# Kernel optimization log

Measured on AMD Instinct MI355X. Metric: run time of the kernel, lower is better.

Reference implementation:

```python
import jax, jax.numpy as jnp
import numpy as np

PAD_ID = 1
NEG = jnp.float32(-1e30)


def setup_inputs() -> dict:
    key = jax.random.key(0)
    ks = jax.random.split(key, 12)
    T, B, S, D, E, V = 20, 32, 400, 512, 512, 50000
    s = 0.02  # weight init scale for numerical sanity
    return {
        "inputs": jax.random.randint(ks[0], (T, B), 0, V),
        "src": jax.random.randint(ks[1], (S, B, 1), 0, V),
        "h_e": jax.random.normal(ks[2], (S, B, D), jnp.float32),
        "h0": jnp.zeros((B, D), jnp.float32),
        "c0": jnp.zeros((B, D), jnp.float32),
        "W_emb": jax.random.normal(ks[3], (V, E), jnp.float32) * s,
        "W_proj": jax.random.normal(ks[4], (E, 3 * D), jnp.float32) * s,
        "b_out": jax.random.normal(ks[5], (V,), jnp.float32) * s,
        "proj_u_W": jax.random.normal(ks[6], (1, 3 * D), jnp.float32) * s,
        "proj_u_b": jnp.zeros((1,), jnp.float32),
        "enc_W": jax.random.normal(ks[7], (D, D), jnp.float32) * s,
        "dec_W": jax.random.normal(ks[8], (D, D), jnp.float32) * s,
        "W_ih": jax.random.normal(ks[9], (4 * D, E), jnp.float32) * s,
        "W_hh": jax.random.normal(ks[10], (4 * D, D), jnp.float32) * s,
        "b_ih": jnp.zeros((4 * D,), jnp.float32),
        "b_hh": jnp.zeros((4 * D,), jnp.float32),
    }


def reference(inputs, src, h_e, h0, c0, W_emb, W_proj, b_out, proj_u_W,
              proj_u_b, enc_W, dec_W, W_ih, W_hh, b_ih, b_hh):
    T, B = inputs.shape
    D = h0.shape[1]
    V = W_emb.shape[0]
    src_bs = src[:, :, 0].T                       # [B, S]
    # Sect 2.4 shared output weights: W_out = tanh(W_emb @ W_proj)  [V, 3D]
    W_out = jnp.tanh(W_emb @ W_proj)
    rows = jnp.arange(B)[:, None]
    tpos = jnp.arange(T)

    def step(carry, xs):
        h, c, hist = carry                        # hist: [T, B, D] decoder-state history
        inp_t, t = xs
        emb = W_emb[inp_t]                        # [B, E]
        # single-layer LSTM cell (torch gate order i, f, g, o)
        gates = emb @ W_ih.T + h @ W_hh.T + b_ih + b_hh
        i, f, g, o = jnp.split(gates, 4, axis=-1)
        c_new = jax.nn.sigmoid(f) * c + jax.nn.sigmoid(i) * jnp.tanh(g)
        hd = jax.nn.sigmoid(o) * jnp.tanh(c_new)  # [B, D]
        # encoder intra-attention
        q = hd @ enc_W.T
        ae = jax.nn.softmax(jnp.einsum('bd,sbd->bs', q, h_e), axis=-1)  # [B, S]
        ce = jnp.einsum('bs,sbd->bd', ae, h_e)
        # decoder intra-attention over steps < t (zero context at t==0)
        qd = hd @ dec_W.T
        sd = jnp.einsum('bd,tbd->bt', qd, hist)
        sd = jnp.where(tpos[None, :] < t, sd, NEG)
        ad = jax.nn.softmax(sd, axis=-1)
        cd = jnp.where(t > 0, jnp.einsum('bt,tbd->bd', ad, hist), 0.0)
        hist = hist.at[t].set(hd)
        # pointer-generator
        ccat = jnp.concatenate([hd, ce, cd], axis=-1)        # [B, 3D]
        logits = ccat @ W_out.T + b_out                      # [B, V]
        logits = logits.at[:, PAD_ID].set(NEG)
        p_gen = jax.nn.softmax(logits, axis=-1)
        p_switch = jax.nn.sigmoid(ccat @ proj_u_W.T + proj_u_b)  # [B, 1]
        # copy distribution: scatter attention into vocab
        copy = jnp.zeros((B, V), logits.dtype).at[rows, src_bs].add(ae)
        scores = copy * p_switch + p_gen * (1.0 - p_switch)
        return (hd, c_new, hist), scores

    hist0 = jnp.zeros((T, B, D), h0.dtype)
    _, scores = jax.lax.scan(step, (h0, c0, hist0), (inputs, tpos))
    return scores  # [T, B, V]
```

## Files before the change

### kernel.cpp

```cpp
#include <hip/hip_runtime.h>
#include <stdint.h>

typedef unsigned short u16;
typedef unsigned int   u32;

using f32x4 = __attribute__((ext_vector_type(4))) float;
using s16x8 = __attribute__((ext_vector_type(8))) short;

#define TT 20
#define BB 32
#define SS 400
#define DD 512
#define VV 50000
#define VP2 50176

__device__ __forceinline__ float bf2f(u16 u){
  u32 x = ((u32)u) << 16;
  return __builtin_bit_cast(float, x);
}
__device__ __forceinline__ u16 f2bf(float f){
  u32 x = __builtin_bit_cast(u32, f);
  x = x + 0x7fffu + ((x >> 16) & 1u);
  return (u16)(x >> 16);
}
__device__ __forceinline__ float sigm(float x){ return 1.0f/(1.0f + __expf(-x)); }
__device__ __forceinline__ float tanh_fast(float x){
  float a = fabsf(x);
  if (a < 0.25f){ float x2 = x*x; return x + x*x2*(-0.33333334f + 0.13333334f*x2); }
  return tanhf(x);
}
__device__ __forceinline__ void gld16(const void* g, void* l){
  __builtin_amdgcn_global_load_lds((const __attribute__((address_space(1))) void*)g,
                                   (__attribute__((address_space(3))) void*)l, 16, 0, 0);
}

__global__ __launch_bounds__(256) void k_prep(
    const float* __restrict__ W_proj,
    const float* __restrict__ W_ih,   const float* __restrict__ W_hh,
    const float* __restrict__ b_ih,   const float* __restrict__ b_hh,
    const float* __restrict__ h0,     const float* __restrict__ c0,
    const float* __restrict__ enc_W,  const float* __restrict__ dec_W,
    u16* __restrict__ WpT,
    u16* __restrict__ Wihs, u16* __restrict__ Whhs,
    u16* __restrict__ encWb, u16* __restrict__ decWb, float* __restrict__ bgs,
    float* __restrict__ hist, u16* __restrict__ histb, float* __restrict__ c_st,
    float* __restrict__ psE)
{
  int i = blockIdx.x*256 + threadIdx.x;
  if (i < 1280){ psE[i] = 0.0f; return; }
  i -= 1280;
  if (i < 2048){ int d = i >> 2, g = i & 3; bgs[i] = b_ih[g*512 + d] + b_hh[g*512 + d]; return; }
  i -= 2048;
  if (i < 16384){ float hv = h0[i]; hist[i] = hv; histb[i] = f2bf(hv); c_st[i] = c0[i]; return; }
  i -= 16384;
  if (i < 786432){ int j = i >> 9, k = i & 511; WpT[i] = f2bf(W_proj[k*1536 + j]); return; }
  i -= 786432;
  if (i < 1048576){
    int mp = i >> 9, k = i & 511; int d = mp >> 2, g = mp & 3;
    Wihs[i] = f2bf(W_ih[(size_t)(g*512 + d)*512 + k]); return; }
  i -= 1048576;
  if (i < 1048576){
    int mp = i >> 9, k = i & 511; int d = mp >> 2, g = mp & 3;
    Whhs[i] = f2bf(W_hh[(size_t)(g*512 + d)*512 + k]); return; }
  i -= 1048576;
  if (i < 262144){ encWb[i] = f2bf(enc_W[i]); return; }
  i -= 262144;
  if (i < 262144){ decWb[i] = f2bf(dec_W[i]); return; }
}

__global__ __launch_bounds__(256) void k_cast_emb(const float* __restrict__ in, u16* __restrict__ out){
  int i = blockIdx.x*256 + threadIdx.x;
  int base = i*4;
  if (base >= VP2*DD) return;
  uint2 o;
  if (base < VV*DD){
    float4 v = *(const float4*)&in[base];
    o.x = (u32)f2bf(v.x) | ((u32)f2bf(v.y) << 16);
    o.y = (u32)f2bf(v.z) | ((u32)f2bf(v.w) << 16);
  } else { o.x = 0u; o.y = 0u; }
  *(uint2*)&out[base] = o;
}

__global__ __launch_bounds__(256) void k_cast_he(const float* __restrict__ in, u16* __restrict__ out){
  int i = blockIdx.x*256 + threadIdx.x;
  int base = i*4;
  if (base >= SS*BB*DD) return;
  const int s = base >> 14;
  const int b = (base >> 9) & 31;
  const int d = base & 511;
  float4 v = *(const float4*)&in[base];
  uint2 o;
  o.x = (u32)f2bf(v.x) | ((u32)f2bf(v.y) << 16);
  o.y = (u32)f2bf(v.z) | ((u32)f2bf(v.w) << 16);
  *(uint2*)&out[((size_t)(b*SS + s) << 9) + d] = o;
}

__global__ __launch_bounds__(256) void k_gather(const int* __restrict__ inp,
                                                const u16* __restrict__ Wb, u16* __restrict__ out){
  int i = blockIdx.x*256 + threadIdx.x;
  if (i >= TT*BB*DD) return;
  int r = i >> 9, k = i & 511;
  out[i] = Wb[(size_t)inp[r]*DD + k];
}

template<int EPI>
__device__ __forceinline__ void gemm_tile(
    const u16* __restrict__ A, const u16* __restrict__ B,
    float* __restrict__ Cf, u16* __restrict__ Cb, const float* __restrict__ bias,
    int K, int mt, int nt, int ldc, int nmax, char* smemc)
{
  u16* As = (u16*)smemc;
  u16* Bs = (u16*)(smemc + 16384);
  const int tid = threadIdx.x;
  const int w = tid >> 6, l = tid & 63;
  const int m0 = mt*128, n0 = nt*128;
  const int srow = tid >> 3;
  const int scol = ((tid & 7) ^ ((tid >> 3) & 7)) * 8;
  const int wm = (w >> 1)*64, wn = (w & 1)*64;
  const int fr = l & 15;
  const int g4 = l >> 4;
  f32x4 acc[4][4] = {};
  for (int k0 = 0; k0 < K; k0 += 64){
    #pragma unroll
    for (int j = 0; j < 4; ++j){
      gld16(A + (size_t)(m0 + j*32 + srow)*K + k0 + scol, (char*)As + j*4096 + (w << 10));
      gld16(B + (size_t)(n0 + j*32 + srow)*K + k0 + scol, (char*)Bs + j*4096 + (w << 10));
    }
    __syncthreads();
    #pragma unroll
    for (int h = 0; h < 2; ++h){
      s16x8 af[4], bfr[4];
      #pragma unroll
      for (int i = 0; i < 4; ++i){
        const int ra = wm + i*16 + fr;
        af[i]  = *(const s16x8*)((char*)As + ra*128 + ((((h << 2) + g4) ^ (ra & 7)) << 4));
        const int rb = wn + i*16 + fr;
        bfr[i] = *(const s16x8*)((char*)Bs + rb*128 + ((((h << 2) + g4) ^ (rb & 7)) << 4));
      }
      #pragma unroll
      for (int i = 0; i < 4; ++i)
        #pragma unroll
        for (int j2 = 0; j2 < 4; ++j2)
          acc[i][j2] = __builtin_amdgcn_mfma_f32_16x16x32_bf16(af[i], bfr[j2], acc[i][j2], 0, 0, 0);
    }
    __syncthreads();
  }
  #pragma unroll
  for (int i = 0; i < 4; ++i){
    #pragma unroll
    for (int j = 0; j < 4; ++j){
      #pragma unroll
      for (int r = 0; r < 4; ++r){
        const int row = m0 + wm + i*16 + (l >> 4)*4 + r;
        const int col = n0 + wn + j*16 + fr;
        const float v = acc[i][j][r];
        if constexpr (EPI == 0){ Cf[(size_t)row*ldc + col] = v; }
        else if constexpr (EPI == 1){ Cb[(size_t)row*ldc + col] = f2bf(tanh_fast(v)); }
        else { if (col < nmax) Cb[(size_t)row*ldc + col] = f2bf(v + bias[col]); }
      }
    }
  }
}

template<int EPI, int ORD>
__global__ __launch_bounds__(256) void gemm_bt(
    const u16* __restrict__ A, const u16* __restrict__ B,
    float* __restrict__ Cf, u16* __restrict__ Cb, const float* __restrict__ bias,
    int K, int TM, int TN, int ldc, int nmax)
{
  __shared__ __align__(16) char smem[32768];
  int bid = blockIdx.x;
  if (ORD >= 1){
    const int n = TM*TN, x = bid & 7, i = bid >> 3;
    const int q = n >> 3, r = n & 7;
    bid = (x < r ? x*(q+1) : r*(q+1) + (x-r)*q) + i;
  }
  const int mt = (ORD == 1) ? bid / TN : bid % TM;
  const int nt = (ORD == 1) ? bid % TN : bid / TM;
  gemm_tile<EPI>(A, B, Cf, Cb, bias, K, mt, nt, ldc, nmax, smem);
}

__global__ __launch_bounds__(256) void k_lstm(
    const u16* __restrict__ Whhs, const float* __restrict__ X, const float* __restrict__ bgs,
    float* __restrict__ hist, u16* __restrict__ histb, float* __restrict__ c_st,
    u16* __restrict__ ccatb, int t)
{
  __shared__ __align__(16) u16 Hs[32*512];
  __shared__ __align__(16) u16 As[16*512];
  __shared__ float Cp[4][16][32];
  const int blk = blockIdx.x;
  const int tid = threadIdx.x;
  const int w = tid >> 6, l = tid & 63;
  const char* hsrc = (const char*)(histb + (size_t)t*16384);
  #pragma unroll
  for (int p = 0; p < 8; ++p)
    gld16(hsrc + p*4096 + w*1024 + l*16, (char*)Hs + p*4096 + w*1024);
  const char* asrc = (const char*)(Whhs + (size_t)blk*16*512);
  #pragma unroll
  for (int p = 0; p < 4; ++p)
    gld16(asrc + p*4096 + w*1024 + l*16, (char*)As + p*4096 + w*1024);
  __syncthreads();
  {
    const int fr = l & 15, fko = (l >> 4)*8;
    f32x4 acc0 = {}, acc1 = {};
    #pragma unroll
    for (int kk = 0; kk < 4; ++kk){
      const int kb = (w*4 + kk)*32;
      s16x8 af = *(const s16x8*)&As[fr*512 + kb + fko];
      s16x8 b0 = *(const s16x8*)&Hs[fr*512 + kb + fko];
      s16x8 b1 = *(const s16x8*)&Hs[(16 + fr)*512 + kb + fko];
      acc0 = __builtin_amdgcn_mfma_f32_16x16x32_bf16(af, b0, acc0, 0, 0, 0);
      acc1 = __builtin_amdgcn_mfma_f32_16x16x32_bf16(af, b1, acc1, 0, 0, 0);
    }
    #pragma unroll
    for (int r = 0; r < 4; ++r){
      Cp[w][(l >> 4)*4 + r][fr]      = acc0[r];
      Cp[w][(l >> 4)*4 + r][16 + fr] = acc1[r];
    }
  }
  __syncthreads();
  if (tid < 128){
    const int dl = tid >> 5, b = tid & 31;
    const int d = blk*4 + dl;
    const int bd = b*512 + d;
    float gv[4];
    #pragma unroll
    for (int g = 0; g < 4; ++g)
      gv[g] = Cp[0][dl*4 + g][b] + Cp[1][dl*4 + g][b] + Cp[2][dl*4 + g][b] + Cp[3][dl*4 + g][b];
    const float4 x4 = *(const float4*)&X[((size_t)(t*BB + b))*2048 + d*4];
    const float4 g4 = *(const float4*)&bgs[d*4];
    const float iv = gv[0] + x4.x + g4.x;
    const float fv = gv[1] + x4.y + g4.y;
    const float gg = gv[2] + x4.z + g4.z;
    const float ov = gv[3] + x4.w + g4.w;
    const float cn = sigm(fv)*c_st[bd] + sigm(iv)*tanhf(gg);
    const float hd = sigm(ov)*tanhf(cn);
    c_st[bd] = cn;
    hist[(size_t)(t + 1)*16384 + bd] = hd;
    const u16 hb = f2bf(hd);
    histb[(size_t)(t + 1)*16384 + bd] = hb;
    ccatb[((size_t)(t*BB + b))*1536 + d] = hb;
  }
}

__global__ __launch_bounds__(256) void k_bulkq(
    const u16* __restrict__ Hb, const u16* __restrict__ encWb, const u16* __restrict__ decWb,
    float* __restrict__ qe_all, float* __restrict__ qd_all)
{
  __shared__ __align__(16) char smem[32768];
  const int e = blockIdx.x;
  const int which = e / 20;
  const int e2 = e % 20;
  const int mt = e2 % 5, nt = e2 / 5;
  gemm_tile<0>(Hb, which ? decWb : encWb, which ? qd_all : qe_all,
               nullptr, nullptr, 512, mt, nt, 512, 0, smem);
}

__global__ __launch_bounds__(256) void k_attn(
    const u16* __restrict__ heb, const float* __restrict__ hist,
    const float* __restrict__ qe_all, const float* __restrict__ qd_all,
    const float* __restrict__ puW,
    u16* __restrict__ ccatb, float* __restrict__ aeall,
    float* __restrict__ psE, float* __restrict__ psD)
{
  __shared__ float hcur[512];
  __shared__ float qv[512];
  __shared__ float ael[SS];
  __shared__ float red[256];
  __shared__ float part[4*512];
  __shared__ float adl[TT];
  __shared__ float sdl[TT];
  __shared__ float shs[2];
  const int blk = blockIdx.x;
  const int tid = threadIdx.x;

  if (blk < 640){
    const int row = blk;
    const int t = row >> 5, b = row & 31;
    const float* hsrc = hist + (size_t)(t + 1)*16384 + b*512;
    const float* qsrc = qe_all + (size_t)row*512;
    hcur[tid] = hsrc[tid]; hcur[tid + 256] = hsrc[tid + 256];
    qv[tid] = qsrc[tid];   qv[tid + 256] = qsrc[tid + 256];
    __syncthreads();
    for (int pass = 0; pass < 7; ++pass){
      const int s = pass*64 + (tid >> 2);
      if (s < SS){
        const u16* gp = heb + ((size_t)(b*SS + s))*512 + (tid & 3)*128;
        const float* hp = qv + (tid & 3)*128;
        float p = 0.0f;
        #pragma unroll 4
        for (int k8 = 0; k8 < 128; k8 += 8){
          s16x8 g8 = *(const s16x8*)&gp[k8];
          #pragma unroll
          for (int q = 0; q < 8; ++q) p += bf2f((u16)g8[q])*hp[k8 + q];
        }
        p += __shfl_xor(p, 1); p += __shfl_xor(p, 2);
        if ((tid & 3) == 0) ael[s] = p;
      }
    }
    __syncthreads();
    float lm = -1e30f;
    for (int s = tid; s < SS; s += 256) lm = fmaxf(lm, ael[s]);
    red[tid] = lm; __syncthreads();
    for (int st = 128; st; st >>= 1){ if (tid < st) red[tid] = fmaxf(red[tid], red[tid + st]); __syncthreads(); }
    const float M = red[0]; __syncthreads();
    float ls = 0.0f;
    for (int s = tid; s < SS; s += 256){ float p = __expf(ael[s] - M); ael[s] = p; ls += p; }
    red[tid] = ls; __syncthreads();
    for (int st = 128; st; st >>= 1){ if (tid < st) red[tid] += red[tid + st]; __syncthreads(); }
    const float inv = 1.0f/red[0];
    __syncthreads();
    {
      const int g = tid >> 6, th = tid & 63;
      const int d0 = th*8;
      float a8[8] = {};
      for (int s = g; s < SS; s += 4){
        const float a = ael[s];
        s16x8 hv = *(const s16x8*)&heb[((size_t)(b*SS + s))*512 + d0];
        #pragma unroll
        for (int q = 0; q < 8; ++q) a8[q] += a*bf2f((u16)hv[q]);
      }
      *(float4*)&part[g*512 + d0]     = float4{a8[0], a8[1], a8[2], a8[3]};
      *(float4*)&part[g*512 + d0 + 4] = float4{a8[4], a8[5], a8[6], a8[7]};
    }
    __syncthreads();
    {
      const int dd = tid*2;
      float ce0 = part[dd]     + part[512 + dd]     + part[1024 + dd]     + part[1536 + dd];
      float ce1 = part[dd + 1] + part[512 + dd + 1] + part[1024 + dd + 1] + part[1536 + dd + 1];
      ce0 *= inv; ce1 *= inv;
      *(u32*)&ccatb[(size_t)row*1536 + 512 + dd] = (u32)f2bf(ce0) | ((u32)f2bf(ce1) << 16);
      float pv = hcur[dd]*puW[dd] + hcur[dd + 1]*puW[dd + 1]
               + ce0*puW[512 + dd] + ce1*puW[512 + dd + 1];
      red[tid] = pv;
    }
    __syncthreads();
    for (int st = 128; st; st >>= 1){ if (tid < st) red[tid] += red[tid + st]; __syncthreads(); }
    if (tid == 0) psE[row] = red[0];
    for (int s = tid; s < SS; s += 256) aeall[(size_t)row*SS + s] = ael[s]*inv;
  } else {
    const int row = blk - 640;
    const int t = row >> 5, b = row & 31;
    const float* qsrc = qd_all + (size_t)row*512;
    qv[tid] = qsrc[tid]; qv[tid + 256] = qsrc[tid + 256];
    __syncthreads();
    for (int u0 = 0; u0 < t; u0 += 8){
      const int u = u0 + (tid >> 5);
      if (u < t){
        const float* hu = hist + (size_t)(u + 1)*16384 + b*512;
        float p = 0.0f;
        #pragma unroll
        for (int j = 0; j < 4; ++j){
          const int kb = (tid & 31)*4 + j*128;
          const float4 h4 = *(const float4*)&hu[kb];
          const float4 q4 = *(const float4*)&qv[kb];
          p += h4.x*q4.x + h4.y*q4.y + h4.z*q4.z + h4.w*q4.w;
        }
        p += __shfl_xor(p, 1); p += __shfl_xor(p, 2); p += __shfl_xor(p, 4);
        p += __shfl_xor(p, 8); p += __shfl_xor(p, 16);
        if ((tid & 31) == 0) sdl[u] = p;
      }
    }
    __syncthreads();
    if (tid == 0 && t > 0){
      float m2 = -1e30f;
      for (int u = 0; u < t; ++u) m2 = fmaxf(m2, sdl[u]);
      float s2 = 0.0f;
      for (int u = 0; u < t; ++u){ float p = __expf(sdl[u] - m2); adl[u] = p; s2 += p; }
      shs[0] = 1.0f/s2;
    }
    __syncthreads();
    const float invd = (t > 0) ? shs[0] : 0.0f;
    const int d0 = tid*2;
    float e0 = 0.0f, e1 = 0.0f;
    for (int u = 0; u < t; ++u){
      const float a = adl[u];
      const float* hu = hist + (size_t)(u + 1)*16384 + b*512 + d0;
      e0 += a*hu[0]; e1 += a*hu[1];
    }
    e0 *= invd; e1 *= invd;
    *(u32*)&ccatb[(size_t)row*1536 + 1024 + d0] = (u32)f2bf(e0) | ((u32)f2bf(e1) << 16);
    float pv = e0*puW[1024 + d0] + e1*puW[1024 + d0 + 1];
    red[tid] = pv; __syncthreads();
    for (int st = 128; st; st >>= 1){ if (tid < st) red[tid] += red[tid + st]; __syncthreads(); }
    if (tid == 0) psD[row] = red[0];
  }
}

__global__ __launch_bounds__(256) void k_softmax(
    const u16* __restrict__ lg, float* __restrict__ out,
    const float* __restrict__ psE, const float* __restrict__ psD, const float* __restrict__ puB,
    const int* __restrict__ src, const float* __restrict__ ae_all)
{
  const int r = blockIdx.x, tid = threadIdx.x;
  __shared__ float rm[256], rs[256];
  const u16* row = lg + (size_t)r*VP2;
  float m = -1e30f, s = 0.0f;
  for (int v8 = tid*8; v8 < VV; v8 += 2048){
    uint4 pk = *(const uint4*)&row[v8];
    u32 wds[4] = {pk.x, pk.y, pk.z, pk.w};
    #pragma unroll
    for (int q = 0; q < 8; ++q){
      if (v8 + q == 1) continue;
      float x = bf2f((u16)((wds[q >> 1] >> ((q & 1)*16)) & 0xffffu));
      if (x > m){ s = s*__expf(m - x) + 1.0f; m = x; }
      else s += __expf(x - m);
    }
  }
  rm[tid] = m; rs[tid] = s; __syncthreads();
  for (int st = 128; st; st >>= 1){
    if (tid < st){
      float m2 = fmaxf(rm[tid], rm[tid + st]);
      rs[tid] = rs[tid]*__expf(rm[tid] - m2) + rs[tid + st]*__expf(rm[tid + st] - m2);
      rm[tid] = m2;
    }
    __syncthreads();
  }
  const float M = rm[0];
  const float ps = 1.0f/(1.0f + __expf(-(psE[r] + psD[r] + puB[0])));
  const float inv = (1.0f - ps)/rs[0];
  float* orow = out + (size_t)r*VV;
  for (int v8 = tid*8; v8 < VV; v8 += 2048){
    uint4 pk = *(const uint4*)&row[v8];
    u32 wds[4] = {pk.x, pk.y, pk.z, pk.w};
    float o[8];
    #pragma unroll
    for (int q = 0; q < 8; ++q){
      float x = bf2f((u16)((wds[q >> 1] >> ((q & 1)*16)) & 0xffffu));
      o[q] = (v8 + q == 1) ? 0.0f : __expf(x - M)*inv;
    }
    *(float4*)&orow[v8]     = float4{o[0], o[1], o[2], o[3]};
    *(float4*)&orow[v8 + 4] = float4{o[4], o[5], o[6], o[7]};
  }
  __syncthreads();
  const int b = r & 31;
  for (int sp = tid; sp < SS; sp += 256){
    const int v = src[sp*BB + b];
    atomicAdd(&orow[v], ae_all[(size_t)r*SS + sp]*ps);
  }
}

extern "C" void kernel_launch(void* const* d_in, const int* in_sizes, int n_in,
                              void* d_out, int out_size, void* d_ws, size_t ws_size,
                              hipStream_t stream)
{
  const int*   inputs = (const int*)  d_in[0];
  const int*   src    = (const int*)  d_in[1];
  const float* h_e    = (const float*)d_in[2];
  const float* h0     = (const float*)d_in[3];
  const float* c0     = (const float*)d_in[4];
  const float* W_emb  = (const float*)d_in[5];
  const float* W_proj = (const float*)d_in[6];
  const float* b_out  = (const float*)d_in[7];
  const float* puW    = (const float*)d_in[8];
  const float* puB    = (const float*)d_in[9];
  const float* enc_W  = (const float*)d_in[10];
  const float* dec_W  = (const float*)d_in[11];
  const float* W_ih   = (const float*)d_in[12];
  const float* W_hh   = (const float*)d_in[13];
  const float* b_ih   = (const float*)d_in[14];
  const float* b_hh   = (const float*)d_in[15];
  float* out = (float*)d_out;

  char* wp = (char*)d_ws;
  auto alloc = [&](size_t bytes) -> char* {
    char* p = wp; wp += (bytes + 255) & ~(size_t)255; return p;
  };
  u16*   Wembb = (u16*)  alloc((size_t)VP2*DD*2);
  u16*   WpT   = (u16*)  alloc(1536*512*2);
  u16*   heb   = (u16*)  alloc((size_t)SS*BB*DD*2);
  u16*   logitsb = (u16*)Wembb;
  u16*   Woutb = (u16*)  alloc((size_t)VP2*1536*2);
  u16*   Wihs  = (u16*)  alloc(2048*512*2);
  u16*   Whhs  = (u16*)  alloc(2048*512*2);
  u16*   encWb = (u16*)  alloc(512*512*2);
  u16*   decWb = (u16*)  alloc(512*512*2);
  float* bgs   = (float*)alloc(2048*4);
  u16*   emba  = (u16*)  alloc((size_t)TT*BB*DD*2);
  float* X     = (float*)alloc((size_t)TT*BB*2048*4);
  float* c_st  = (float*)alloc(BB*DD*4);
  float* hist  = (float*)alloc((size_t)(TT+1)*BB*DD*4);
  u16*   histb = (u16*)  alloc((size_t)(TT+1)*BB*DD*2);
  u16*   ccatb = (u16*)  alloc((size_t)TT*BB*1536*2);
  float* aeall = (float*)alloc((size_t)TT*BB*SS*4);
  float* psE   = (float*)alloc(1280*4);
  float* psD   = psE + 640;
  float* qe_all= (float*)alloc((size_t)TT*BB*DD*4);
  float* qd_all= (float*)alloc((size_t)TT*BB*DD*4);

  k_prep<<<13389, 256, 0, stream>>>(W_proj, W_ih, W_hh, b_ih, b_hh, h0, c0, enc_W, dec_W,
                                    WpT, Wihs, Whhs, encWb, decWb, bgs, hist, histb, c_st, psE);
  k_cast_emb<<<(VP2*DD/4)/256, 256, 0, stream>>>(W_emb, Wembb);
  k_cast_he<<<(SS*BB*DD/4)/256, 256, 0, stream>>>(h_e, heb);
  k_gather<<<(TT*BB*DD + 255)/256, 256, 0, stream>>>(inputs, Wembb, emba);

  gemm_bt<0,0><<<5*16, 256, 0, stream>>>(emba, Wihs, X, nullptr, nullptr, 512, 5, 16, 2048, 0);

  gemm_bt<1,1><<<392*12, 256, 0, stream>>>(Wembb, WpT, nullptr, Woutb, nullptr, 512, 392, 12, 1536, 0);

  for (int t = 0; t < TT; ++t)
    k_lstm<<<128, 256, 0, stream>>>(Whhs, X, bgs, hist, histb, c_st, ccatb, t);

  k_bulkq<<<40, 256, 0, stream>>>(histb + 16384, encWb, decWb, qe_all, qd_all);
  k_attn<<<1280, 256, 0, stream>>>(heb, hist, qe_all, qd_all, puW, ccatb, aeall, psE, psD);

  gemm_bt<3,2><<<5*392, 256, 0, stream>>>(ccatb, Woutb, nullptr, logitsb, b_out, 1536, 5, 392, VP2, VV);

  k_softmax<<<TT*BB, 256, 0, stream>>>(logitsb, out, psE, psD, puB, src, aeall);
}
```

Baseline: 508.3 us.

## Merge prep cast kernels into one launch and stage GEMM epilogue through LDS

Folds the embedding cast, encoder-state cast/transpose and token gather into the single prep kernel. The gather now reads fp32 W_emb directly, so it no longer depends on the cast output. The bf16 GEMM epilogues now write results into shared memory first, then emit 16-byte coalesced row stores, with the bias hoisted into registers. This is meant to cut launch overhead and the scattered 2-byte global stores on the large vocab-output and W_out GEMMs, at the cost of extra LDS (34816 bytes per block) and an additional barrier.

```diff
diff --git a/kernel.cpp b/kernel.cpp
--- a/kernel.cpp
+++ b/kernel.cpp
@@ -40,11 +40,14 @@
     const float* __restrict__ b_ih,   const float* __restrict__ b_hh,
     const float* __restrict__ h0,     const float* __restrict__ c0,
     const float* __restrict__ enc_W,  const float* __restrict__ dec_W,
+    const float* __restrict__ W_emb,  const float* __restrict__ h_e,
+    const int*   __restrict__ inputs,
     u16* __restrict__ WpT,
     u16* __restrict__ Wihs, u16* __restrict__ Whhs,
     u16* __restrict__ encWb, u16* __restrict__ decWb, float* __restrict__ bgs,
     float* __restrict__ hist, u16* __restrict__ histb, float* __restrict__ c_st,
-    float* __restrict__ psE)
+    float* __restrict__ psE,
+    u16* __restrict__ Wembb, u16* __restrict__ heb, u16* __restrict__ emba)
 {
   int i = blockIdx.x*256 + threadIdx.x;
   if (i < 1280){ psE[i] = 0.0f; return; }
@@ -66,41 +69,39 @@
   if (i < 262144){ encWb[i] = f2bf(enc_W[i]); return; }
   i -= 262144;
   if (i < 262144){ decWb[i] = f2bf(dec_W[i]); return; }
-}
-
-__global__ __launch_bounds__(256) void k_cast_emb(const float* __restrict__ in, u16* __restrict__ out){
-  int i = blockIdx.x*256 + threadIdx.x;
-  int base = i*4;
-  if (base >= VP2*DD) return;
-  uint2 o;
-  if (base < VV*DD){
-    float4 v = *(const float4*)&in[base];
+  i -= 262144;
+  if (i < 6422528){
+    int base = i*4;
+    uint2 o;
+    if (base < VV*DD){
+      float4 v = *(const float4*)&W_emb[base];
+      o.x = (u32)f2bf(v.x) | ((u32)f2bf(v.y) << 16);
+      o.y = (u32)f2bf(v.z) | ((u32)f2bf(v.w) << 16);
+    } else { o.x = 0u; o.y = 0u; }
+    *(uint2*)&Wembb[base] = o;
+    return; }
+  i -= 6422528;
+  if (i < 1638400){
+    int base = i*4;
+    const int s = base >> 14;
+    const int b = (base >> 9) & 31;
+    const int d = base & 511;
+    float4 v = *(const float4*)&h_e[base];
+    uint2 o;
     o.x = (u32)f2bf(v.x) | ((u32)f2bf(v.y) << 16);
     o.y = (u32)f2bf(v.z) | ((u32)f2bf(v.w) << 16);
-  } else { o.x = 0u; o.y = 0u; }
-  *(uint2*)&out[base] = o;
-}
-
-__global__ __launch_bounds__(256) void k_cast_he(const float* __restrict__ in, u16* __restrict__ out){
-  int i = blockIdx.x*256 + threadIdx.x;
-  int base = i*4;
-  if (base >= SS*BB*DD) return;
-  const int s = base >> 14;
-  const int b = (base >> 9) & 31;
-  const int d = base & 511;
-  float4 v = *(const float4*)&in[base];
-  uint2 o;
-  o.x = (u32)f2bf(v.x) | ((u32)f2bf(v.y) << 16);
-  o.y = (u32)f2bf(v.z) | ((u32)f2bf(v.w) << 16);
-  *(uint2*)&out[((size_t)(b*SS + s) << 9) + d] = o;
-}
-
-__global__ __launch_bounds__(256) void k_gather(const int* __restrict__ inp,
-                                                const u16* __restrict__ Wb, u16* __restrict__ out){
-  int i = blockIdx.x*256 + threadIdx.x;
-  if (i >= TT*BB*DD) return;
-  int r = i >> 9, k = i & 511;
-  out[i] = Wb[(size_t)inp[r]*DD + k];
+    *(uint2*)&heb[((size_t)(b*SS + s) << 9) + d] = o;
+    return; }
+  i -= 1638400;
+  if (i < 81920){
+    int base = i*4;
+    int r = base >> 9, k = base & 511;
+    float4 v = *(const float4*)&W_emb[(size_t)inputs[r]*DD + k];
+    uint2 o;
+    o.x = (u32)f2bf(v.x) | ((u32)f2bf(v.y) << 16);
+    o.y = (u32)f2bf(v.z) | ((u32)f2bf(v.w) << 16);
+    *(uint2*)&emba[base] = o;
+    return; }
 }
 
 template<int EPI>
@@ -119,6 +120,14 @@
   const int wm = (w >> 1)*64, wn = (w & 1)*64;
   const int fr = l & 15;
   const int g4 = l >> 4;
+  float bv[4];
+  if constexpr (EPI == 3){
+    #pragma unroll
+    for (int j = 0; j < 4; ++j){
+      const int c = n0 + wn + j*16 + fr;
+      bv[j] = (c < nmax) ? bias[c] : 0.0f;
+    }
+  }
   f32x4 acc[4][4] = {};
   for (int k0 = 0; k0 < K; k0 += 64){
     #pragma unroll
@@ -145,18 +154,50 @@
     }
     __syncthreads();
   }
-  #pragma unroll
-  for (int i = 0; i < 4; ++i){
-    #pragma unroll
-    for (int j = 0; j < 4; ++j){
+  if constexpr (EPI == 0){
+    #pragma unroll
+    for (int i = 0; i < 4; ++i)
       #pragma unroll
-      for (int r = 0; r < 4; ++r){
-        const int row = m0 + wm + i*16 + (l >> 4)*4 + r;
-        const int col = n0 + wn + j*16 + fr;
-        const float v = acc[i][j][r];
-        if constexpr (EPI == 0){ Cf[(size_t)row*ldc + col] = v; }
-        else if constexpr (EPI == 1){ Cb[(size_t)row*ldc + col] = f2bf(tanh_fast(v)); }
-        else { if (col < nmax) Cb[(size_t)row*ldc + col] = f2bf(v + bias[col]); }
+      for (int j = 0; j < 4; ++j)
+        #pragma unroll
+        for (int r = 0; r < 4; ++r){
+          const int row = m0 + wm + i*16 + (l >> 4)*4 + r;
+          const int col = n0 + wn + j*16 + fr;
+          Cf[(size_t)row*ldc + col] = acc[i][j][r];
+        }
+  } else {
+    u16* Rs = (u16*)smemc;
+    #pragma unroll
+    for (int i = 0; i < 4; ++i){
+      #pragma unroll
+      for (int j = 0; j < 4; ++j){
+        #pragma unroll
+        for (int r = 0; r < 4; ++r){
+          const int rl = wm + i*16 + (l >> 4)*4 + r;
+          const int cl = wn + j*16 + fr;
+          const float v = acc[i][j][r];
+          u16 o;
+          if constexpr (EPI == 1) o = f2bf(tanh_fast(v));
+          else                    o = f2bf(v + bv[j]);
+          Rs[rl*136 + cl] = o;
+        }
+      }
+    }
+    __syncthreads();
+    const int rr0 = tid >> 4;
+    const int cb  = (tid & 15)*8;
+    #pragma unroll
+    for (int p = 0; p < 8; ++p){
+      const int row = p*16 + rr0;
+      const int gc  = n0 + cb;
+      s16x8 val = *(const s16x8*)&Rs[row*136 + cb];
+      u16* dst = Cb + (size_t)(m0 + row)*ldc + gc;
+      if (EPI == 1 || gc + 8 <= nmax){
+        *(s16x8*)dst = val;
+      } else {
+        #pragma unroll
+        for (int q = 0; q < 8; ++q)
+          if (gc + q < nmax) dst[q] = (u16)val[q];
       }
     }
   }
@@ -168,7 +209,7 @@
     float* __restrict__ Cf, u16* __restrict__ Cb, const float* __restrict__ bias,
     int K, int TM, int TN, int ldc, int nmax)
 {
-  __shared__ __align__(16) char smem[32768];
+  __shared__ __align__(16) char smem[34816];
   int bid = blockIdx.x;
   if (ORD >= 1){
     const int n = TM*TN, x = bid & 7, i = bid >> 3;
@@ -247,7 +288,7 @@
     const u16* __restrict__ Hb, const u16* __restrict__ encWb, const u16* __restrict__ decWb,
     float* __restrict__ qe_all, float* __restrict__ qd_all)
 {
-  __shared__ __align__(16) char smem[32768];
+  __shared__ __align__(16) char smem[34816];
   const int e = blockIdx.x;
   const int which = e / 20;
   const int e2 = e % 20;
@@ -488,11 +529,10 @@
   float* qe_all= (float*)alloc((size_t)TT*BB*DD*4);
   float* qd_all= (float*)alloc((size_t)TT*BB*DD*4);
 
-  k_prep<<<13389, 256, 0, stream>>>(W_proj, W_ih, W_hh, b_ih, b_hh, h0, c0, enc_W, dec_W,
-                                    WpT, Wihs, Whhs, encWb, decWb, bgs, hist, histb, c_st, psE);
-  k_cast_emb<<<(VP2*DD/4)/256, 256, 0, stream>>>(W_emb, Wembb);
-  k_cast_he<<<(SS*BB*DD/4)/256, 256, 0, stream>>>(h_e, heb);
-  k_gather<<<(TT*BB*DD + 255)/256, 256, 0, stream>>>(inputs, Wembb, emba);
+  k_prep<<<45197, 256, 0, stream>>>(W_proj, W_ih, W_hh, b_ih, b_hh, h0, c0, enc_W, dec_W,
+                                    W_emb, h_e, inputs,
+                                    WpT, Wihs, Whhs, encWb, decWb, bgs, hist, histb, c_st, psE,
+                                    Wembb, heb, emba);
 
   gemm_bt<0,0><<<5*16, 256, 0, stream>>>(emba, Wihs, X, nullptr, nullptr, 512, 5, 16, 2048, 0);
 
```

Measured after the change: 495.0 us. 1.03x faster.
